# Performance work log

Hardware: AMD Instinct MI355X
Metric: run time of the kernel (lower is better)

## Reference

```python
import jax, jax.numpy as jnp
import numpy as np

# Last adaptive-conv stage of AdaBIGGAN (BigGAN-128): ch=96 at 128x128, hypernet input dim 148
B, C, H, W, IN = 32, 96, 128, 128, 148


def setup_inputs() -> dict:
    key = jax.random.key(0)
    k0, k1, k2, k3, k4, k5 = jax.random.split(key, 6)
    s = 0.02  # small init scale for hypernetwork linears
    return {
        "h": jax.random.normal(k0, (B, C, H, W), jnp.float32),      # feature map after cond-BN
        "y": jax.random.normal(k1, (B, IN), jnp.float32),           # [shared_embed | z-chunk] cond vector
        "Wg_w": jax.random.normal(k2, (C * C, IN), jnp.float32) * s,  # nn.Linear(148, C*C).weight
        "Wg_b": jax.random.normal(k3, (C * C,), jnp.float32) * s,     # nn.Linear(148, C*C).bias
        "Bg_w": jax.random.normal(k4, (C, IN), jnp.float32) * s,      # nn.Linear(148, C).weight
        "Bg_b": jax.random.normal(k5, (C,), jnp.float32) * s,         # nn.Linear(148, C).bias
    }


def reference(h, y, Wg_w, Wg_b, Bg_w, Bg_b):
    Bn, Cn = h.shape[0], h.shape[1]
    # hypernetwork: per-sample 1x1-conv weight [B, C, C] and bias [B, C]
    w = (y @ Wg_w.T + Wg_b).reshape(Bn, Cn, Cn)
    b = y @ Bg_w.T + Bg_b
    # Faithful to the torch broadcasting: (h[:, :, None] * w[:, :, :, None, None]).sum(2)
    # which collapses exactly to h * w.sum(-1), avoiding the [B,C,C,H,W] blowup.
    scale = w.sum(-1)  # [B, C]
    out = h * scale[:, :, None, None] + b[:, :, None, None]
    return jax.nn.relu(out)  # block.activation1
```

## Files before the change

kernel.cpp:

```cpp
#include <hip/hip_runtime.h>
#include <stdint.h>

#define B_  32
#define C_  96
#define HW_ 16384
#define IN_ 148

typedef float f32x4 __attribute__((ext_vector_type(4)));

__global__ __launch_bounds__(256) void hyper_kernel(
    const float* __restrict__ Wg_w, const float* __restrict__ Wg_b,
    const float* __restrict__ Bg_w, const float* __restrict__ Bg_b,
    const float* __restrict__ y,
    float* __restrict__ scale, float* __restrict__ bias) {
    const int c   = blockIdx.x;
    const int tid = threadIdx.x;

    __shared__ float sW[IN_];
    __shared__ float sB[IN_];
    __shared__ float sWbS;

    if (tid < IN_) {
        float s = 0.f;
        const float* p = Wg_w + (size_t)c * C_ * IN_ + tid;
        #pragma unroll 4
        for (int j = 0; j < C_; ++j) s += p[(size_t)j * IN_];
        sW[tid] = s;
        sB[tid] = Bg_w[c * IN_ + tid];
    }
    if (tid < 64) {
        float v = Wg_b[c * C_ + tid];
        if (tid < C_ - 64) v += Wg_b[c * C_ + 64 + tid];
        #pragma unroll
        for (int off = 32; off > 0; off >>= 1) v += __shfl_down(v, off);
        if (tid == 0) sWbS = v;
    }
    __syncthreads();

    const int wave = tid >> 6, lane = tid & 63;
    for (int b = wave; b < B_; b += 4) {
        float y0 = y[b * IN_ + lane];
        float y1 = y[b * IN_ + 64 + lane];
        float ps = y0 * sW[lane] + y1 * sW[64 + lane];
        float pb = y0 * sB[lane] + y1 * sB[64 + lane];
        if (lane < IN_ - 128) {
            float y2 = y[b * IN_ + 128 + lane];
            ps += y2 * sW[128 + lane];
            pb += y2 * sB[128 + lane];
        }
        #pragma unroll
        for (int off = 32; off > 0; off >>= 1) {
            ps += __shfl_down(ps, off);
            pb += __shfl_down(pb, off);
        }
        if (lane == 0) {
            scale[b * C_ + c] = ps + sWbS;
            bias [b * C_ + c] = pb + Bg_b[c];
        }
    }
}

__global__ __launch_bounds__(256) void apply_kernel(
    const float* __restrict__ h, const float* __restrict__ scale,
    const float* __restrict__ bias, float* __restrict__ out) {
    const int plane = blockIdx.x;
    const float s  = scale[plane];
    const float bb = bias[plane];

    const f32x4* __restrict__ hp =
        reinterpret_cast<const f32x4*>(h) + (size_t)plane * (HW_ / 4) + threadIdx.x;
    f32x4* __restrict__ op =
        reinterpret_cast<f32x4*>(out) + (size_t)plane * (HW_ / 4) + threadIdx.x;

    #pragma unroll
    for (int half = 0; half < 2; ++half) {
        f32x4 v[8];
        #pragma unroll
        for (int i = 0; i < 8; ++i)
            v[i] = __builtin_nontemporal_load(hp + (half * 8 + i) * 256);
        #pragma unroll
        for (int i = 0; i < 8; ++i) {
            f32x4 o;
            o.x = fmaxf(fmaf(v[i].x, s, bb), 0.f);
            o.y = fmaxf(fmaf(v[i].y, s, bb), 0.f);
            o.z = fmaxf(fmaf(v[i].z, s, bb), 0.f);
            o.w = fmaxf(fmaf(v[i].w, s, bb), 0.f);
            __builtin_nontemporal_store(o, op + (half * 8 + i) * 256);
        }
    }
}

extern "C" void kernel_launch(void* const* d_in, const int* in_sizes, int n_in,
                              void* d_out, int out_size, void* d_ws, size_t ws_size,
                              hipStream_t stream) {
    const float* h    = (const float*)d_in[0];
    const float* y    = (const float*)d_in[1];
    const float* Wg_w = (const float*)d_in[2];
    const float* Wg_b = (const float*)d_in[3];
    const float* Bg_w = (const float*)d_in[4];
    const float* Bg_b = (const float*)d_in[5];
    float* out = (float*)d_out;

    float* scale = (float*)d_ws;
    float* bias  = scale + B_ * C_;

    hyper_kernel<<<C_, 256, 0, stream>>>(Wg_w, Wg_b, Bg_w, Bg_b, y, scale, bias);

    apply_kernel<<<B_ * C_, 256, 0, stream>>>(h, scale, bias, out);
}
```

Measured before the change: 344.9 us.

## Fuse hypernetwork reduction into apply kernel with XCD-aware block mapping

Merges the two kernels into one: each block computes its own per-(b,c) scale and bias from the hypernetwork weights, while its first batch of h loads is already in flight. It also remaps block ids so blocks sharing a channel land on the same XCD, keeping the reused Wg_w slice in that XCD's L2. This removes a kernel launch and the dependency between the two kernels, at the cost of every block re-reading and reducing its 96x148 weight slice (32x redundant across the batch).

```diff
diff --git a/kernel.cpp b/kernel.cpp
--- a/kernel.cpp
+++ b/kernel.cpp
@@ -8,85 +8,81 @@
 
 typedef float f32x4 __attribute__((ext_vector_type(4)));
 
-__global__ __launch_bounds__(256) void hyper_kernel(
+__global__ __launch_bounds__(256) void fused_kernel(
+    const float* __restrict__ h, const float* __restrict__ y,
     const float* __restrict__ Wg_w, const float* __restrict__ Wg_b,
     const float* __restrict__ Bg_w, const float* __restrict__ Bg_b,
-    const float* __restrict__ y,
-    float* __restrict__ scale, float* __restrict__ bias) {
-    const int c   = blockIdx.x;
+    float* __restrict__ out) {
+    const int bid = blockIdx.x;
+    const int xcd = bid & 7;
+    const int t   = bid >> 3;
+    const int c   = xcd * 12 + (t % 12);
+    const int b   = t / 12;
     const int tid = threadIdx.x;
-
-    __shared__ float sW[IN_];
-    __shared__ float sB[IN_];
-    __shared__ float sWbS;
-
-    if (tid < IN_) {
-        float s = 0.f;
-        const float* p = Wg_w + (size_t)c * C_ * IN_ + tid;
-        #pragma unroll 4
-        for (int j = 0; j < C_; ++j) s += p[(size_t)j * IN_];
-        sW[tid] = s;
-        sB[tid] = Bg_w[c * IN_ + tid];
-    }
-    if (tid < 64) {
-        float v = Wg_b[c * C_ + tid];
-        if (tid < C_ - 64) v += Wg_b[c * C_ + 64 + tid];
-        #pragma unroll
-        for (int off = 32; off > 0; off >>= 1) v += __shfl_down(v, off);
-        if (tid == 0) sWbS = v;
-    }
-    __syncthreads();
-
-    const int wave = tid >> 6, lane = tid & 63;
-    for (int b = wave; b < B_; b += 4) {
-        float y0 = y[b * IN_ + lane];
-        float y1 = y[b * IN_ + 64 + lane];
-        float ps = y0 * sW[lane] + y1 * sW[64 + lane];
-        float pb = y0 * sB[lane] + y1 * sB[64 + lane];
-        if (lane < IN_ - 128) {
-            float y2 = y[b * IN_ + 128 + lane];
-            ps += y2 * sW[128 + lane];
-            pb += y2 * sB[128 + lane];
-        }
-        #pragma unroll
-        for (int off = 32; off > 0; off >>= 1) {
-            ps += __shfl_down(ps, off);
-            pb += __shfl_down(pb, off);
-        }
-        if (lane == 0) {
-            scale[b * C_ + c] = ps + sWbS;
-            bias [b * C_ + c] = pb + Bg_b[c];
-        }
-    }
-}
-
-__global__ __launch_bounds__(256) void apply_kernel(
-    const float* __restrict__ h, const float* __restrict__ scale,
-    const float* __restrict__ bias, float* __restrict__ out) {
-    const int plane = blockIdx.x;
-    const float s  = scale[plane];
-    const float bb = bias[plane];
+    const int plane = b * C_ + c;
 
     const f32x4* __restrict__ hp =
-        reinterpret_cast<const f32x4*>(h) + (size_t)plane * (HW_ / 4) + threadIdx.x;
+        reinterpret_cast<const f32x4*>(h) + (size_t)plane * (HW_ / 4) + tid;
     f32x4* __restrict__ op =
-        reinterpret_cast<f32x4*>(out) + (size_t)plane * (HW_ / 4) + threadIdx.x;
+        reinterpret_cast<f32x4*>(out) + (size_t)plane * (HW_ / 4) + tid;
+
+    f32x4 v[8];
+    #pragma unroll
+    for (int i = 0; i < 8; ++i)
+        v[i] = __builtin_nontemporal_load(hp + i * 256);
+
+    float ps = 0.f, pb = 0.f;
+    if (tid < IN_) {
+        const float* p = Wg_w + (size_t)c * C_ * IN_ + tid;
+        float a0 = 0.f, a1 = 0.f, a2 = 0.f, a3 = 0.f;
+        #pragma unroll 6
+        for (int j = 0; j < C_; j += 4) {
+            a0 += p[(j + 0) * IN_];
+            a1 += p[(j + 1) * IN_];
+            a2 += p[(j + 2) * IN_];
+            a3 += p[(j + 3) * IN_];
+        }
+        const float cs = (a0 + a1) + (a2 + a3);
+        const float yv = y[b * IN_ + tid];
+        ps = yv * cs;
+        pb = yv * Bg_w[c * IN_ + tid];
+    } else if (tid < IN_ + C_) {
+        ps = Wg_b[c * C_ + (tid - IN_)];
+    } else if (tid == IN_ + C_) {
+        pb = Bg_b[c];
+    }
+    #pragma unroll
+    for (int off = 32; off > 0; off >>= 1) {
+        ps += __shfl_xor(ps, off);
+        pb += __shfl_xor(pb, off);
+    }
+    __shared__ float sPS[4], sPB[4];
+    const int wave = tid >> 6, lane = tid & 63;
+    if (lane == 0) { sPS[wave] = ps; sPB[wave] = pb; }
+    __syncthreads();
+    const float s  = (sPS[0] + sPS[1]) + (sPS[2] + sPS[3]);
+    const float bb = (sPB[0] + sPB[1]) + (sPB[2] + sPB[3]);
 
     #pragma unroll
-    for (int half = 0; half < 2; ++half) {
-        f32x4 v[8];
-        #pragma unroll
-        for (int i = 0; i < 8; ++i)
-            v[i] = __builtin_nontemporal_load(hp + (half * 8 + i) * 256);
-        #pragma unroll
-        for (int i = 0; i < 8; ++i) {
-            f32x4 o;
-            o.x = fmaxf(fmaf(v[i].x, s, bb), 0.f);
-            o.y = fmaxf(fmaf(v[i].y, s, bb), 0.f);
-            o.z = fmaxf(fmaf(v[i].z, s, bb), 0.f);
-            o.w = fmaxf(fmaf(v[i].w, s, bb), 0.f);
-            __builtin_nontemporal_store(o, op + (half * 8 + i) * 256);
-        }
+    for (int i = 0; i < 8; ++i) {
+        f32x4 o;
+        o.x = fmaxf(fmaf(v[i].x, s, bb), 0.f);
+        o.y = fmaxf(fmaf(v[i].y, s, bb), 0.f);
+        o.z = fmaxf(fmaf(v[i].z, s, bb), 0.f);
+        o.w = fmaxf(fmaf(v[i].w, s, bb), 0.f);
+        __builtin_nontemporal_store(o, op + i * 256);
+    }
+    #pragma unroll
+    for (int i = 0; i < 8; ++i)
+        v[i] = __builtin_nontemporal_load(hp + (8 + i) * 256);
+    #pragma unroll
+    for (int i = 0; i < 8; ++i) {
+        f32x4 o;
+        o.x = fmaxf(fmaf(v[i].x, s, bb), 0.f);
+        o.y = fmaxf(fmaf(v[i].y, s, bb), 0.f);
+        o.z = fmaxf(fmaf(v[i].z, s, bb), 0.f);
+        o.w = fmaxf(fmaf(v[i].w, s, bb), 0.f);
+        __builtin_nontemporal_store(o, op + (8 + i) * 256);
     }
 }
 
@@ -101,10 +97,5 @@
     const float* Bg_b = (const float*)d_in[5];
     float* out = (float*)d_out;
 
-    float* scale = (float*)d_ws;
-    float* bias  = scale + B_ * C_;
-
-    hyper_kernel<<<C_, 256, 0, stream>>>(Wg_w, Wg_b, Bg_w, Bg_b, y, scale, bias);
-
-    apply_kernel<<<B_ * C_, 256, 0, stream>>>(h, scale, bias, out);
+    fused_kernel<<<B_ * C_, 256, 0, stream>>>(h, y, Wg_w, Wg_b, Bg_w, Bg_b, out);
 }
```

New measurement: 335.7 us. 2.7% less time.
